# Kernel tuning notes

Measured on AMD Instinct MI355X. Metric: run time of the kernel, lower is better.

## Reference

```python
import jax, jax.numpy as jnp
import numpy as np

B, N, GI, GH, GO = 8, 1024, 1024, 128, 128


def _lin_params(k, din, dout):
    # torch.nn.Linear default init: U(-1/sqrt(din), 1/sqrt(din))
    s = 1.0 / np.sqrt(din)
    kw, kb = jax.random.split(k)
    W = jax.random.uniform(kw, (din, dout), jnp.float32, -s, s)
    b = jax.random.uniform(kb, (dout,), jnp.float32, -s, s)
    return W, b


def setup_inputs() -> dict:
    key = jax.random.key(0)
    ks = jax.random.split(key, 6)
    aa_rep = jax.random.normal(ks[0], (B, N, GI), dtype=jnp.float32)
    rpa = jax.random.randint(ks[1], (B, N, N), 0, 2).astype(jnp.int32)
    W_in, b_in = _lin_params(ks[2], GI, GH)
    W_h0, b_h0 = _lin_params(ks[3], GH, GH)
    W_h1, b_h1 = _lin_params(ks[4], GH, GH)
    W_out, b_out = _lin_params(ks[5], GH, GO)
    return dict(aa_rep=aa_rep, rpa=rpa, W_in=W_in, b_in=b_in,
                W_h0=W_h0, b_h0=b_h0, W_h1=W_h1, b_h1=b_h1,
                W_out=W_out, b_out=b_out)


def _norm_adj(rpa):
    # get_graph_edge: edges = nonzero(rpa) minus self-loops; GCNConv then
    # re-adds self-loops and applies symmetric deg^{-1/2} normalization.
    n = rpa.shape[-1]
    A = (rpa != 0).astype(jnp.float32)
    eye = jnp.eye(n, dtype=jnp.float32)
    A = A * (1.0 - eye) + eye  # [B,N,N] A_hat = A (no diag) + I
    deg = A.sum(-1)  # [B,N], includes self-loop
    dinv = jnp.where(deg > 0, 1.0 / jnp.sqrt(deg), 0.0)
    return A * dinv[..., :, None] * dinv[..., None, :]


def reference(aa_rep, rpa, W_in, b_in, W_h0, b_h0, W_h1, b_h1, W_out, b_out):
    Ahat = _norm_adj(rpa)  # [B,N,N]

    def gcn(h, W, b):
        # GCNConv: aggregate(normalized) of (h @ W), then bias; model applies relu
        return jax.nn.relu(jnp.einsum('bij,bjd->bid', Ahat, h @ W) + b)

    h1 = gcn(aa_rep, W_in, b_in)   # layer_in
    h2 = gcn(h1, W_h0, b_h0)       # hidden 0
    h3 = gcn(h2, W_h1, b_h1)       # hidden 1
    h4 = gcn(h3, W_out, b_out)     # layer_out
    # mean over stacked layer outputs reps[1:]
    return (h1 + h2 + h3 + h4) * 0.25
```

## Files before the change

kernel.cpp:

```cpp
#include <hip/hip_runtime.h>
#include <hip/hip_bf16.h>

typedef __bf16 bf16;
typedef __bf16 bf16x4 __attribute__((ext_vector_type(4)));
typedef __bf16 bf16x8 __attribute__((ext_vector_type(8)));
typedef float f32x4 __attribute__((ext_vector_type(4)));

#define NN 1024
#define GH 128
#define MROWS 8192

static __device__ __forceinline__ f32x4 mfma16(bf16x8 a, bf16x8 b, f32x4 c) {
    return __builtin_amdgcn_mfma_f32_16x16x32_bf16(a, b, c, 0, 0, 0);
}

__global__ __launch_bounds__(256) void wtrans0_kernel(const float* __restrict__ W0,
                                                      bf16* __restrict__ T0) {
    int t = blockIdx.x * 256 + threadIdx.x;
    int n = t & 127, k0 = (t >> 7) * 8;
    bf16x8 o;
#pragma unroll
    for (int ii = 0; ii < 8; ++ii) o[ii] = (bf16)W0[(size_t)(k0 + ii) * GH + n];
    *reinterpret_cast<bf16x8*>(T0 + (size_t)n * NN + k0) = o;
}

__global__ __launch_bounds__(512, 4) void prep_gemm_kernel(
        const int* __restrict__ rpa, const float* __restrict__ aa,
        const float* __restrict__ W1, const float* __restrict__ W2, const float* __restrict__ W3,
        const bf16* __restrict__ Wt0,
        unsigned char* __restrict__ A01b, float* __restrict__ dinv,
        bf16* __restrict__ T1, bf16* __restrict__ T2, bf16* __restrict__ T3,
        bf16* __restrict__ Yt) {
    __shared__ bf16 Alds[32768];
    int bid = blockIdx.x, tid = threadIdx.x;
    if (bid < 1024) {
        int rb = (bid & 7) * 128 + (bid >> 3);
        int wave = tid >> 6, lane = tid & 63;
        int row = rb * 8 + wave;
        int i = row & (NN - 1);
        const int4* p = reinterpret_cast<const int4*>(rpa + (size_t)row * NN);
        unsigned char* brow = A01b + (size_t)row * 128;
        int cnt = 0;
#pragma unroll
        for (int it = 0; it < 4; ++it) {
            int4 v = p[lane + it * 64];
            int j = (lane + it * 64) * 4;
            int a0 = (v.x != 0), a1 = (v.y != 0), a2 = (v.z != 0), a3 = (v.w != 0);
            cnt += (a0 & (j + 0 != i)) + (a1 & (j + 1 != i)) +
                   (a2 & (j + 2 != i)) + (a3 & (j + 3 != i));
            unsigned nib = (unsigned)(a0 | (j + 0 == i))
                         | ((unsigned)(a1 | (j + 1 == i)) << 1)
                         | ((unsigned)(a2 | (j + 2 == i)) << 2)
                         | ((unsigned)(a3 | (j + 3 == i)) << 3);
            unsigned pn = __shfl_xor(nib, 1, 64);
            if (!(lane & 1))
                brow[it * 32 + (lane >> 1)] = (unsigned char)(nib | (pn << 4));
        }
#pragma unroll
        for (int off = 32; off > 0; off >>= 1) cnt += __shfl_down(cnt, off, 64);
        if (lane == 0) dinv[row] = rsqrtf((float)(cnt + 1));
        if (tid < 6) {
            int t = bid * 6 + tid;
            const float* W; bf16* T; int local;
            if (t < 2048)      { W = W1; T = T1; local = t; }
            else if (t < 4096) { W = W2; T = T2; local = t - 2048; }
            else               { W = W3; T = T3; local = t - 4096; }
            int n = local & 127, k0 = (local >> 7) * 8;
            bf16x8 o;
#pragma unroll
            for (int ii = 0; ii < 8; ++ii) o[ii] = (bf16)W[(size_t)(k0 + ii) * GH + n];
            *reinterpret_cast<bf16x8*>(T + (size_t)n * GH + k0) = o;
        }
    } else {
        int g = bid - 1024;
        int wave = tid >> 6, lane = tid & 63;
        int lrow = lane & 15, lg = lane >> 4;
        int lb = (g & 7) * 32 + (g >> 3);
        int m0 = lb * 32;
#pragma unroll
        for (int i = 0; i < 8; ++i) {
            int idx = i * 512 + tid;
            int row = idx >> 7, u = idx & 127;
            const float* src = aa + (size_t)(m0 + row) * NN + u * 8;
            float4 f0 = *reinterpret_cast<const float4*>(src);
            float4 f1 = *reinterpret_cast<const float4*>(src + 4);
            bf16x8 v;
            v[0] = (bf16)f0.x; v[1] = (bf16)f0.y; v[2] = (bf16)f0.z; v[3] = (bf16)f0.w;
            v[4] = (bf16)f1.x; v[5] = (bf16)f1.y; v[6] = (bf16)f1.z; v[7] = (bf16)f1.w;
            *reinterpret_cast<bf16x8*>(&Alds[(row * 128 + (u ^ (row & 7))) * 8]) = v;
        }
        __syncthreads();
        int c0 = wave * 16;
        const bf16* Bp = Wt0 + (size_t)(c0 + lrow) * NN + lg * 8;
        f32x4 acc[2][2] = {};
#pragma unroll
        for (int f = 0; f < 32; ++f) {
            bf16x8 bb = *reinterpret_cast<const bf16x8*>(Bp + f * 32);
            int u = f * 4 + lg;
#pragma unroll
            for (int rg = 0; rg < 2; ++rg) {
                int r = rg * 16 + lrow;
                bf16x8 a = *reinterpret_cast<const bf16x8*>(&Alds[(r * 128 + (u ^ (r & 7))) * 8]);
                acc[rg][f & 1] = mfma16(a, bb, acc[rg][f & 1]);
            }
        }
        int rl = lg * 4;
        int col = c0 + lrow;
#pragma unroll
        for (int rg = 0; rg < 2; ++rg) {
            f32x4 s = acc[rg][0] + acc[rg][1];
            int rbase = m0 + rg * 16 + rl;
            bf16x4 o;
            o[0] = (bf16)s[0]; o[1] = (bf16)s[1]; o[2] = (bf16)s[2]; o[3] = (bf16)s[3];
            *reinterpret_cast<bf16x4*>(Yt + (size_t)col * MROWS + rbase) = o;
        }
    }
}

template <int MODE, bool HASW, bool DSCALE>
__global__ __launch_bounds__(512, 4) void fused3_kernel(const unsigned char* __restrict__ A01b,
                                                        const bf16* __restrict__ Xt,
                                                        const bf16* __restrict__ Wt,
                                                        const float* __restrict__ dinv,
                                                        const float* __restrict__ bias,
                                                        bf16* __restrict__ Hst,
                                                        float* __restrict__ outp) {
    __shared__ bf16 Alds[16384];
    __shared__ bf16 Ths[4096];
    __shared__ bf16 Tls[4096];
    int tid = threadIdx.x;
    int wave = tid >> 6, lane = tid & 63;
    int lrow = lane & 15, lg = lane >> 4;
    int lb = (blockIdx.x & 7) * 32 + (blockIdx.x >> 3);
    int m0 = lb * 32;
    int b = blockIdx.x & 7;
    int c0 = wave * 16;
    const bf16* Bp = Xt + (size_t)(c0 + lrow) * MROWS + b * NN + lg * 8;
    f32x4 acc[2][2] = {};
    int erow = tid >> 4;
    int eub  = (tid & 15) * 4;
    int ers  = erow & 7;
#pragma unroll
    for (int h = 0; h < 2; ++h) {
        if (h) __syncthreads();
        {
            unsigned w = *reinterpret_cast<const unsigned*>(
                A01b + (size_t)(m0 + erow) * 128 + h * 64 + eub);
#pragma unroll
            for (int i = 0; i < 4; ++i) {
                unsigned byte = (w >> (8 * i)) & 0xffu;
                bf16x8 v;
                if constexpr (DSCALE) {
                    const float* dq = dinv + b * NN + (h * 64 + eub + i) * 8;
                    float4 q0 = *reinterpret_cast<const float4*>(dq);
                    float4 q1 = *reinterpret_cast<const float4*>(dq + 4);
                    v[0] = (byte & 1u)   ? (bf16)q0.x : (bf16)0.f;
                    v[1] = (byte & 2u)   ? (bf16)q0.y : (bf16)0.f;
                    v[2] = (byte & 4u)   ? (bf16)q0.z : (bf16)0.f;
                    v[3] = (byte & 8u)   ? (bf16)q0.w : (bf16)0.f;
                    v[4] = (byte & 16u)  ? (bf16)q1.x : (bf16)0.f;
                    v[5] = (byte & 32u)  ? (bf16)q1.y : (bf16)0.f;
                    v[6] = (byte & 64u)  ? (bf16)q1.z : (bf16)0.f;
                    v[7] = (byte & 128u) ? (bf16)q1.w : (bf16)0.f;
                } else {
#pragma unroll
                    for (int k = 0; k < 8; ++k) v[k] = ((byte >> k) & 1u) ? (bf16)1.f : (bf16)0.f;
                }
                *reinterpret_cast<bf16x8*>(&Alds[(erow * 64 + ((eub + i) ^ ers)) * 8]) = v;
            }
        }
        __syncthreads();
#pragma unroll
        for (int fl = 0; fl < 16; ++fl) {
            int f = h * 16 + fl;
            bf16x8 bb = *reinterpret_cast<const bf16x8*>(Bp + f * 32);
            int ul = fl * 4 + lg;
#pragma unroll
            for (int rg = 0; rg < 2; ++rg) {
                int r = rg * 16 + lrow;
                bf16x8 a = *reinterpret_cast<const bf16x8*>(&Alds[(r * 64 + (ul ^ (r & 7))) * 8]);
                acc[rg][f & 1] = mfma16(a, bb, acc[rg][f & 1]);
            }
        }
    }
    int rl = lg * 4;

    if constexpr (!HASW) {
#pragma unroll
        for (int rg = 0; rg < 2; ++rg) {
            f32x4 s = acc[rg][0] + acc[rg][1];
            int rbase = m0 + rg * 16 + rl;
            float4 d4 = *reinterpret_cast<const float4*>(&dinv[rbase]);
            int col = c0 + lrow;
            float bv = bias[col];
            float v0 = fmaxf(s[0] * d4.x + bv, 0.f);
            float v1 = fmaxf(s[1] * d4.y + bv, 0.f);
            float v2 = fmaxf(s[2] * d4.z + bv, 0.f);
            float v3 = fmaxf(s[3] * d4.w + bv, 0.f);
            float* op = outp + (size_t)rbase * GH + col;
            if (MODE == 0) {
                op[0] = 0.25f * v0; op[GH] = 0.25f * v1;
                op[2 * GH] = 0.25f * v2; op[3 * GH] = 0.25f * v3;
            } else {
                op[0] += 0.25f * v0; op[GH] += 0.25f * v1;
                op[2 * GH] += 0.25f * v2; op[3 * GH] += 0.25f * v3;
            }
            if (MODE != 2) {
                bf16x4 h4;
                h4[0] = (bf16)(v0 * d4.x); h4[1] = (bf16)(v1 * d4.y);
                h4[2] = (bf16)(v2 * d4.z); h4[3] = (bf16)(v3 * d4.w);
                *reinterpret_cast<bf16x4*>(Hst + (size_t)col * MROWS + rbase) = h4;
            }
        }
    } else {
        __syncthreads();
        {
            int tcol = c0 + lrow;
#pragma unroll
            for (int rg = 0; rg < 2; ++rg) {
                f32x4 s = acc[rg][0] + acc[rg][1];
#pragma unroll
                for (int r = 0; r < 4; ++r) {
                    int trow = rg * 16 + rl + r;
                    float tv = s[r];
                    bf16 hi = (bf16)tv;
                    int ei = trow * 128 + (tcol ^ ((trow & 7) << 3));
                    Ths[ei] = hi;
                    Tls[ei] = (bf16)(tv - (float)hi);
                }
            }
        }
        __syncthreads();
        f32x4 u[2] = {};
        int wcol = c0 + lrow;
#pragma unroll
        for (int ks = 0; ks < 4; ++ks) {
            int e0 = ks * 32 + lg * 8;
            bf16x8 wv = *reinterpret_cast<const bf16x8*>(Wt + (size_t)wcol * GH + e0);
#pragma unroll
            for (int rg = 0; rg < 2; ++rg) {
                int trow2 = rg * 16 + lrow;
                int te = trow2 * 128 + (e0 ^ ((trow2 & 7) << 3));
                bf16x8 thi = *reinterpret_cast<const bf16x8*>(&Ths[te]);
                bf16x8 tlo = *reinterpret_cast<const bf16x8*>(&Tls[te]);
                u[rg] = mfma16(thi, wv, u[rg]);
                u[rg] = mfma16(tlo, wv, u[rg]);
            }
        }
#pragma unroll
        for (int rg = 0; rg < 2; ++rg) {
            int rbase = m0 + rg * 16 + rl;
            float4 d4 = *reinterpret_cast<const float4*>(&dinv[rbase]);
            float bv = bias[wcol];
            float v0 = fmaxf(u[rg][0] * d4.x + bv, 0.f);
            float v1 = fmaxf(u[rg][1] * d4.y + bv, 0.f);
            float v2 = fmaxf(u[rg][2] * d4.z + bv, 0.f);
            float v3 = fmaxf(u[rg][3] * d4.w + bv, 0.f);
            float* op = outp + (size_t)rbase * GH + wcol;
            if (MODE == 0) {
                op[0] = 0.25f * v0; op[GH] = 0.25f * v1;
                op[2 * GH] = 0.25f * v2; op[3 * GH] = 0.25f * v3;
            } else {
                op[0] += 0.25f * v0; op[GH] += 0.25f * v1;
                op[2 * GH] += 0.25f * v2; op[3 * GH] += 0.25f * v3;
            }
            if (MODE != 2) {
                bf16x4 h4;
                h4[0] = (bf16)(v0 * d4.x); h4[1] = (bf16)(v1 * d4.y);
                h4[2] = (bf16)(v2 * d4.z); h4[3] = (bf16)(v3 * d4.w);
                *reinterpret_cast<bf16x4*>(Hst + (size_t)wcol * MROWS + rbase) = h4;
            }
        }
    }
}

extern "C" void kernel_launch(void* const* d_in, const int* in_sizes, int n_in,
                              void* d_out, int out_size, void* d_ws, size_t ws_size,
                              hipStream_t stream) {
    const float* aa    = (const float*)d_in[0];
    const int*   rpa   = (const int*)d_in[1];
    const float* W_in  = (const float*)d_in[2];
    const float* b_in  = (const float*)d_in[3];
    const float* W_h0  = (const float*)d_in[4];
    const float* b_h0  = (const float*)d_in[5];
    const float* W_h1  = (const float*)d_in[6];
    const float* b_h1  = (const float*)d_in[7];
    const float* W_out = (const float*)d_in[8];
    const float* b_out = (const float*)d_in[9];
    float* out = (float*)d_out;

    char* ws = (char*)d_ws;
    size_t off = 0;
    float* dinv = (float*)(ws + off); off += (size_t)MROWS * 4;
    unsigned char* A01b = (unsigned char*)(ws + off); off += (size_t)MROWS * 128;
    bf16*  Yt   = (bf16*)(ws + off);  off += (size_t)GH * MROWS * 2;
    bf16*  HstA = (bf16*)(ws + off);  off += (size_t)GH * MROWS * 2;
    bf16*  HstB = (bf16*)(ws + off);  off += (size_t)GH * MROWS * 2;
    bf16*  Wt0  = (bf16*)(ws + off);  off += (size_t)GH * NN * 2;
    bf16*  Wt1  = (bf16*)(ws + off);  off += (size_t)GH * GH * 2;
    bf16*  Wt2  = (bf16*)(ws + off);  off += (size_t)GH * GH * 2;
    bf16*  Wt3  = (bf16*)(ws + off);  off += (size_t)GH * GH * 2;

    wtrans0_kernel<<<64, 256, 0, stream>>>(W_in, Wt0);
    prep_gemm_kernel<<<1280, 512, 0, stream>>>(rpa, aa, W_h0, W_h1, W_out, Wt0,
                                               A01b, dinv, Wt1, Wt2, Wt3, Yt);
    fused3_kernel<0, false, true><<<256, 512, 0, stream>>>(A01b, Yt,   Wt1, dinv, b_in,  HstA, out);
    fused3_kernel<1, true, false><<<256, 512, 0, stream>>>(A01b, HstA, Wt1, dinv, b_h0, HstB, out);
    fused3_kernel<1, true, false><<<256, 512, 0, stream>>>(A01b, HstB, Wt2, dinv, b_h1, HstA, out);
    fused3_kernel<2, true, false><<<256, 512, 0, stream>>>(A01b, HstA, Wt3, dinv, b_out, HstB, out);
}
```

Before: 88.70 us.

## Interleave prep and GEMM blocks and halve GEMM LDS via K-split staging

The prep/GEMM kernel now interleaves block roles so every fifth block runs the input-projection GEMM and the other four do adjacency packing. Previously all packing blocks ran first and all GEMM blocks after them. The GEMM stages the fp32-to-bf16 A tile in two K halves, which halves shared memory to 32KB. Each thread now loads contiguous 128-byte runs, and an extra barrier is added between the halves. The aim is more resident blocks per CU and a mix of memory-bound and MFMA work running concurrently, at the cost of one more sync per GEMM block.

```diff
diff --git a/kernel.cpp b/kernel.cpp
--- a/kernel.cpp
+++ b/kernel.cpp
@@ -31,12 +31,12 @@
         unsigned char* __restrict__ A01b, float* __restrict__ dinv,
         bf16* __restrict__ T1, bf16* __restrict__ T2, bf16* __restrict__ T3,
         bf16* __restrict__ Yt) {
-    __shared__ bf16 Alds[32768];
+    __shared__ bf16 Alds[16384];
     int bid = blockIdx.x, tid = threadIdx.x;
-    if (bid < 1024) {
-        int rb = (bid & 7) * 128 + (bid >> 3);
-        int wave = tid >> 6, lane = tid & 63;
-        int row = rb * 8 + wave;
+    int wave = tid >> 6, lane = tid & 63;
+    if (bid % 5 != 0) {
+        int j = bid - bid / 5 - 1;
+        int row = j * 8 + wave;
         int i = row & (NN - 1);
         const int4* p = reinterpret_cast<const int4*>(rpa + (size_t)row * NN);
         unsigned char* brow = A01b + (size_t)row * 128;
@@ -44,14 +44,14 @@
 #pragma unroll
         for (int it = 0; it < 4; ++it) {
             int4 v = p[lane + it * 64];
-            int j = (lane + it * 64) * 4;
+            int jj = (lane + it * 64) * 4;
             int a0 = (v.x != 0), a1 = (v.y != 0), a2 = (v.z != 0), a3 = (v.w != 0);
-            cnt += (a0 & (j + 0 != i)) + (a1 & (j + 1 != i)) +
-                   (a2 & (j + 2 != i)) + (a3 & (j + 3 != i));
-            unsigned nib = (unsigned)(a0 | (j + 0 == i))
-                         | ((unsigned)(a1 | (j + 1 == i)) << 1)
-                         | ((unsigned)(a2 | (j + 2 == i)) << 2)
-                         | ((unsigned)(a3 | (j + 3 == i)) << 3);
+            cnt += (a0 & (jj + 0 != i)) + (a1 & (jj + 1 != i)) +
+                   (a2 & (jj + 2 != i)) + (a3 & (jj + 3 != i));
+            unsigned nib = (unsigned)(a0 | (jj + 0 == i))
+                         | ((unsigned)(a1 | (jj + 1 == i)) << 1)
+                         | ((unsigned)(a2 | (jj + 2 == i)) << 2)
+                         | ((unsigned)(a3 | (jj + 3 == i)) << 3);
             unsigned pn = __shfl_xor(nib, 1, 64);
             if (!(lane & 1))
                 brow[it * 32 + (lane >> 1)] = (unsigned char)(nib | (pn << 4));
@@ -60,7 +60,7 @@
         for (int off = 32; off > 0; off >>= 1) cnt += __shfl_down(cnt, off, 64);
         if (lane == 0) dinv[row] = rsqrtf((float)(cnt + 1));
         if (tid < 6) {
-            int t = bid * 6 + tid;
+            int t = j * 6 + tid;
             const float* W; bf16* T; int local;
             if (t < 2048)      { W = W1; T = T1; local = t; }
             else if (t < 4096) { W = W2; T = T2; local = t - 2048; }
@@ -72,36 +72,43 @@
             *reinterpret_cast<bf16x8*>(T + (size_t)n * GH + k0) = o;
         }
     } else {
-        int g = bid - 1024;
-        int wave = tid >> 6, lane = tid & 63;
+        int g = bid / 5;
         int lrow = lane & 15, lg = lane >> 4;
-        int lb = (g & 7) * 32 + (g >> 3);
+        int lb = (bid & 7) * 32 + (g >> 3);
         int m0 = lb * 32;
-#pragma unroll
-        for (int i = 0; i < 8; ++i) {
-            int idx = i * 512 + tid;
-            int row = idx >> 7, u = idx & 127;
-            const float* src = aa + (size_t)(m0 + row) * NN + u * 8;
-            float4 f0 = *reinterpret_cast<const float4*>(src);
-            float4 f1 = *reinterpret_cast<const float4*>(src + 4);
-            bf16x8 v;
-            v[0] = (bf16)f0.x; v[1] = (bf16)f0.y; v[2] = (bf16)f0.z; v[3] = (bf16)f0.w;
-            v[4] = (bf16)f1.x; v[5] = (bf16)f1.y; v[6] = (bf16)f1.z; v[7] = (bf16)f1.w;
-            *reinterpret_cast<bf16x8*>(&Alds[(row * 128 + (u ^ (row & 7))) * 8]) = v;
-        }
-        __syncthreads();
         int c0 = wave * 16;
         const bf16* Bp = Wt0 + (size_t)(c0 + lrow) * NN + lg * 8;
         f32x4 acc[2][2] = {};
-#pragma unroll
-        for (int f = 0; f < 32; ++f) {
-            bf16x8 bb = *reinterpret_cast<const bf16x8*>(Bp + f * 32);
-            int u = f * 4 + lg;
-#pragma unroll
-            for (int rg = 0; rg < 2; ++rg) {
-                int r = rg * 16 + lrow;
-                bf16x8 a = *reinterpret_cast<const bf16x8*>(&Alds[(r * 128 + (u ^ (r & 7))) * 8]);
-                acc[rg][f & 1] = mfma16(a, bb, acc[rg][f & 1]);
+        int arow = tid >> 4;
+        int au   = (tid & 15) * 4;
+        int ars  = arow & 7;
+#pragma unroll
+        for (int h = 0; h < 2; ++h) {
+            if (h) __syncthreads();
+            {
+                const float* src = aa + (size_t)(m0 + arow) * NN + h * 512 + au * 8;
+#pragma unroll
+                for (int i = 0; i < 4; ++i) {
+                    float4 f0 = *reinterpret_cast<const float4*>(src + i * 8);
+                    float4 f1 = *reinterpret_cast<const float4*>(src + i * 8 + 4);
+                    bf16x8 v;
+                    v[0] = (bf16)f0.x; v[1] = (bf16)f0.y; v[2] = (bf16)f0.z; v[3] = (bf16)f0.w;
+                    v[4] = (bf16)f1.x; v[5] = (bf16)f1.y; v[6] = (bf16)f1.z; v[7] = (bf16)f1.w;
+                    *reinterpret_cast<bf16x8*>(&Alds[(arow * 64 + ((au + i) ^ ars)) * 8]) = v;
+                }
+            }
+            __syncthreads();
+#pragma unroll
+            for (int fl = 0; fl < 16; ++fl) {
+                int f = h * 16 + fl;
+                bf16x8 bb = *reinterpret_cast<const bf16x8*>(Bp + f * 32);
+                int ul = fl * 4 + lg;
+#pragma unroll
+                for (int rg = 0; rg < 2; ++rg) {
+                    int r = rg * 16 + lrow;
+                    bf16x8 a = *reinterpret_cast<const bf16x8*>(&Alds[(r * 64 + (ul ^ (r & 7))) * 8]);
+                    acc[rg][f & 1] = mfma16(a, bb, acc[rg][f & 1]);
+                }
             }
         }
         int rl = lg * 4;
```

New measurement: 98.31 us. +10.8%, slower.
